# Performance work log

Hardware: AMD Instinct MI355X
Metric: run time of the kernel (lower is better)

The kernel has to match this reference:

```python
import jax, jax.numpy as jnp
import numpy as np

EMBED_DIM = 1024
NUM_HEADS = 16
HEAD_DIM = EMBED_DIM // NUM_HEADS
SCALE = HEAD_DIM ** -0.5


def setup_inputs() -> dict:
    key = jax.random.key(0)
    ks = jax.random.split(key, 12)
    B, S, D = 4, 2048, EMBED_DIM
    x = jax.random.normal(ks[0], (B, S, D), dtype=jnp.float32)
    key_padding_mask = jax.random.randint(ks[1], (B, S), 0, 2).astype(jnp.bool_)
    init = 1.0 / np.sqrt(D)
    def lin(kw, kb):
        W = jax.random.uniform(kw, (D, D), minval=-init, maxval=init, dtype=jnp.float32)
        b = jax.random.uniform(kb, (D,), minval=-init, maxval=init, dtype=jnp.float32)
        return W, b
    Wq, bq = lin(ks[2], ks[3])
    Wk, bk = lin(ks[4], ks[5])
    Wv, bv = lin(ks[6], ks[7])
    Wo, bo = lin(ks[8], ks[9])
    return {"x": x, "key_padding_mask": key_padding_mask,
            "Wq": Wq, "bq": bq, "Wk": Wk, "bk": bk,
            "Wv": Wv, "bv": bv, "Wo": Wo, "bo": bo}


def reference(x, key_padding_mask, Wq, bq, Wk, bk, Wv, bv, Wo, bo):
    B, S, D = x.shape
    H, Hd = NUM_HEADS, HEAD_DIM
    # projections (torch Linear: y = x @ W.T + b)
    q = (x @ Wq.T + bq).reshape(B, S, H, Hd).transpose(0, 2, 1, 3)  # [B,H,S,Hd]
    k = (x @ Wk.T + bk).reshape(B, S, H, Hd).transpose(0, 2, 1, 3)
    v = (x @ Wv.T + bv).reshape(B, S, H, Hd).transpose(0, 2, 1, 3)
    scores = jnp.einsum('bhqd,bhkd->bhqk', q, k) * SCALE  # [B,H,S,S]
    mask = key_padding_mask[:, None, None, :]  # [B,1,1,S]
    scores = jnp.where(mask, -jnp.inf, scores)
    probs = jax.nn.softmax(scores, axis=-1)
    # dropout p=0.0 (inference) -> identity
    out = jnp.einsum('bhqk,bhkd->bhqd', probs, v)  # [B,H,S,Hd]
    out = out.transpose(0, 2, 1, 3).reshape(B, S, D)
    return out @ Wo.T + bo
```

## Files before the change

### kernel.cpp

```cpp
#include <hip/hip_runtime.h>
#include <stdint.h>

typedef __bf16 bf16;
typedef __bf16 bf16x8 __attribute__((ext_vector_type(8)));
typedef float f32x4 __attribute__((ext_vector_type(4)));

#define SEQ 2048
#define NHEAD 16
#define HDIM 64
#define DMODEL 1024
#define NBATCH 4
#define ATT_SCALE 0.18033688011112042f
#define SEQHD (SEQ * HDIM)
#define BHSTRIDE (2 * SEQHD)


__device__ __forceinline__ void gload_lds16(const bf16* g, bf16* l) {
  __builtin_amdgcn_global_load_lds(
      (const __attribute__((address_space(1))) uint32_t*)g,
      (__attribute__((address_space(3))) uint32_t*)l, 16, 0, 0);
}

__device__ __forceinline__ uint32_t pk2(float a, float b) {
  bf16 x = (bf16)a, y = (bf16)b;
  return (uint32_t)__builtin_bit_cast(uint16_t, x) |
         ((uint32_t)__builtin_bit_cast(uint16_t, y) << 16);
}

__global__ __launch_bounds__(256) void cvt_kernel(const float* __restrict__ src,
                                                  bf16* __restrict__ dst) {
  size_t i = ((size_t)blockIdx.x * 256 + threadIdx.x) * 16;
#pragma unroll
  for (int j = 0; j < 2; ++j) {
    float4 f0 = *(const float4*)(src + i + j * 8);
    float4 f1 = *(const float4*)(src + i + j * 8 + 4);
    bf16x8 v;
    v[0] = (bf16)f0.x; v[1] = (bf16)f0.y; v[2] = (bf16)f0.z; v[3] = (bf16)f0.w;
    v[4] = (bf16)f1.x; v[5] = (bf16)f1.y; v[6] = (bf16)f1.z; v[7] = (bf16)f1.w;
    *(bf16x8*)(dst + i + j * 8) = v;
  }
}

__global__ __launch_bounds__(256) void cvt3_kernel(const float* __restrict__ a,
                                                   const float* __restrict__ b,
                                                   const float* __restrict__ c,
                                                   bf16* __restrict__ dst) {
  const float* s = blockIdx.y == 0 ? a : (blockIdx.y == 1 ? b : c);
  bf16* d = dst + (size_t)blockIdx.y * DMODEL * DMODEL;
  size_t i = ((size_t)blockIdx.x * 256 + threadIdx.x) * 16;
#pragma unroll
  for (int j = 0; j < 2; ++j) {
    float4 f0 = *(const float4*)(s + i + j * 8);
    float4 f1 = *(const float4*)(s + i + j * 8 + 4);
    bf16x8 v;
    v[0] = (bf16)f0.x; v[1] = (bf16)f0.y; v[2] = (bf16)f0.z; v[3] = (bf16)f0.w;
    v[4] = (bf16)f1.x; v[5] = (bf16)f1.y; v[6] = (bf16)f1.z; v[7] = (bf16)f1.w;
    *(bf16x8*)(d + i + j * 8) = v;
  }
}

__global__ __launch_bounds__(256) void scan_kernel(int* __restrict__ posv,
                                                   int* __restrict__ inv) {
  __shared__ int sums[256];
  const int b = blockIdx.x, t = threadIdx.x;
  int* m = posv + b * SEQ;
  int* iv = inv + b * SEQ;
  int f[8], cnt = 0;
#pragma unroll
  for (int j = 0; j < 8; ++j) {
    int x = m[t * 8 + j];
    int unm = (x < 0) ? 0 : ((x & 0x40000000) ? 1 : (x == 0 ? 1 : 0));
    f[j] = unm; cnt += unm;
    iv[t * 8 + j] = 0;
  }
  sums[t] = cnt;
  __syncthreads();
  if (t == 0) {
    int acc = 0;
#pragma unroll 8
    for (int i = 0; i < 256; ++i) { int s = sums[i]; sums[i] = acc; acc += s; }
  }
  __syncthreads();
  int p = sums[t];
#pragma unroll
  for (int j = 0; j < 8; ++j) {
    m[t * 8 + j] = (int)((f[j] ? 0x40000000u : 0x80000000u) | (unsigned)p);
    if (f[j]) iv[p] = t * 8 + j;
    p += f[j];
  }
}

__global__ __launch_bounds__(256) void qproj_kernel(
    const bf16* __restrict__ xb, const bf16* __restrict__ Wall,
    const float* __restrict__ bq, bf16* __restrict__ Qall) {
  __shared__ __align__(16) bf16 lW[64 * 64];
  __shared__ __align__(16) bf16 lXw[4][32 * 64];
  const int t = threadIdx.x, wave = t >> 6, lane = t & 63;
  const int quad = lane >> 4, c = lane & 15;
  const int m0 = blockIdx.x * 128;
  const int h = blockIdx.y;
  const bf16* W = Wall + (size_t)(h * HDIM) * DMODEL;
  bf16* pw = lXw[wave];
  const int sr = lane >> 3, sg = lane & 7;
  const bf16* aS = xb + (size_t)(m0 + wave * 32 + sr) * DMODEL + ((sg ^ sr) * 8);
  const bf16* wS = W + (size_t)(wave * 8 + sr) * DMODEL + ((sg ^ sr) * 8);
  f32x4 acc[2][4] = {};
  for (int k0 = 0; k0 < DMODEL; k0 += 64) {
    __syncthreads();
    gload_lds16(wS + k0, lW + wave * 512);
    gload_lds16(wS + 32 * DMODEL + k0, lW + wave * 512 + 2048);
#pragma unroll
    for (int ii = 0; ii < 4; ++ii)
      gload_lds16(aS + k0 + (size_t)ii * 8 * DMODEL, pw + ii * 512);
    __syncthreads();
#pragma unroll
    for (int kk = 0; kk < 2; ++kk) {
      bf16x8 af[2], bfr[4];
#pragma unroll
      for (int mi = 0; mi < 2; ++mi) {
        int row = mi * 16 + c;
        af[mi] = *(const bf16x8*)(pw + row * 64 + (((kk * 4 + quad) ^ (row & 7)) * 8));
      }
#pragma unroll
      for (int ni = 0; ni < 4; ++ni) {
        int row = ni * 16 + c;
        bfr[ni] = *(const bf16x8*)(lW + row * 64 + (((kk * 4 + quad) ^ (row & 7)) * 8));
      }
#pragma unroll
      for (int mi = 0; mi < 2; ++mi)
#pragma unroll
        for (int ni = 0; ni < 4; ++ni)
          acc[mi][ni] = __builtin_amdgcn_mfma_f32_16x16x32_bf16(af[mi], bfr[ni], acc[mi][ni], 0, 0, 0);
    }
  }
#pragma unroll
  for (int ni = 0; ni < 4; ++ni) {
    int hd = ni * 16 + c;
    float bqv = bq[h * HDIM + hd];
#pragma unroll
    for (int mi = 0; mi < 2; ++mi)
#pragma unroll
      for (int r = 0; r < 4; ++r) {
        int tok = m0 + wave * 32 + mi * 16 + quad * 4 + r;
        int b = tok >> 11, s = tok & 2047;
        Qall[((size_t)(b * NHEAD + h) * SEQ + s) * HDIM + hd] =
            (bf16)((acc[mi][ni][r] + bqv) * ATT_SCALE);
      }
  }
}

__global__ __launch_bounds__(256) void kvproj_kernel(
    const bf16* __restrict__ xb, const bf16* __restrict__ Wall,
    const float* __restrict__ bk, const float* __restrict__ bv,
    const int* __restrict__ posv, const int* __restrict__ inv,
    bf16* __restrict__ kv) {
  __shared__ __align__(16) bf16 lW[64 * 64];
  __shared__ __align__(16) bf16 lXw[4][32 * 64];
  const int t = threadIdx.x, wave = t >> 6, lane = t & 63;
  const int quad = lane >> 4, c = lane & 15;
  const int bx = blockIdx.x;
  const int b_loc = bx >> 4, mb = bx & 15;
  const int nt = blockIdx.y;
  const int isV = nt >> 4, h = nt & 15;
  int v2 = posv[b_loc * SEQ + SEQ - 1];
  int nk = (v2 & 0x3FFFFFFF) + (v2 >= 0 ? 1 : 0);
  const int c0 = mb * 128;
  if (c0 >= nk) return;
  const bf16* W = Wall + (size_t)(1 + isV) * DMODEL * DMODEL + (size_t)(h * HDIM) * DMODEL;
  const float* bias = (isV ? bv : bk) + h * HDIM;
  bf16* pw = lXw[wave];
  const int sr = lane >> 3, sg = lane & 7;
  const int swzc = (sg ^ sr) * 8;
  const bf16* wS = W + (size_t)(wave * 8 + sr) * DMODEL + swzc;
  const int* invb = inv + b_loc * SEQ;
  int grow[4];
#pragma unroll
  for (int ii = 0; ii < 4; ++ii)
    grow[ii] = invb[c0 + wave * 32 + ii * 8 + sr];
  const bf16* xbb = xb + (size_t)b_loc * SEQ * DMODEL + swzc;
  f32x4 acc[2][4] = {};
  for (int k0 = 0; k0 < DMODEL; k0 += 64) {
    __syncthreads();
    gload_lds16(wS + k0, lW + wave * 512);
    gload_lds16(wS + 32 * DMODEL + k0, lW + wave * 512 + 2048);
#pragma unroll
    for (int ii = 0; ii < 4; ++ii)
      gload_lds16(xbb + (size_t)grow[ii] * DMODEL + k0, pw + ii * 512);
    __syncthreads();
#pragma unroll
    for (int kk = 0; kk < 2; ++kk) {
      bf16x8 af[2], bfr[4];
#pragma unroll
      for (int mi = 0; mi < 2; ++mi) {
        int row = mi * 16 + c;
        af[mi] = *(const bf16x8*)(pw + row * 64 + (((kk * 4 + quad) ^ (row & 7)) * 8));
      }
#pragma unroll
      for (int ni = 0; ni < 4; ++ni) {
        int row = ni * 16 + c;
        bfr[ni] = *(const bf16x8*)(lW + row * 64 + (((kk * 4 + quad) ^ (row & 7)) * 8));
      }
#pragma unroll
      for (int mi = 0; mi < 2; ++mi)
#pragma unroll
        for (int ni = 0; ni < 4; ++ni)
          acc[mi][ni] = __builtin_amdgcn_mfma_f32_16x16x32_bf16(af[mi], bfr[ni], acc[mi][ni], 0, 0, 0);
    }
  }
  bf16* base = kv + (size_t)(b_loc * NHEAD + h) * BHSTRIDE;
#pragma unroll
  for (int ni = 0; ni < 4; ++ni) {
    int hd = ni * 16 + c;
    float bv_ = bias[hd];
#pragma unroll
    for (int mi = 0; mi < 2; ++mi)
#pragma unroll
      for (int r = 0; r < 4; ++r) {
        int dst = c0 + wave * 32 + mi * 16 + quad * 4 + r;
        float val = acc[mi][ni][r] + bv_;
        if (isV) base[SEQHD + (size_t)hd * SEQ + dst] = (bf16)val;
        else     base[(size_t)dst * HDIM + hd] = (bf16)val;
      }
  }
}

__global__ __launch_bounds__(256) void zf_kernel(bf16* __restrict__ kv,
                                                 const int* __restrict__ posv) {
  const int bh = blockIdx.x, t = threadIdx.x;
  const int b_loc = bh >> 4, h = bh & 15;
  int v2 = posv[b_loc * SEQ + SEQ - 1];
  int nk = (v2 & 0x3FFFFFFF) + (v2 >= 0 ? 1 : 0);
  int NT = ((nk + 63) >> 6) << 6;
  int pad = NT - nk;
  if (pad == 0) return;
  bf16* base = kv + (size_t)(b_loc * NHEAD + h) * BHSTRIDE;
  int hd = t & 63;
  for (int rr = t >> 6; rr < pad; rr += 4) {
    base[(size_t)(nk + rr) * HDIM + hd] = (bf16)0.0f;
    base[SEQHD + (size_t)hd * SEQ + nk + rr] = (bf16)0.0f;
  }
}

__global__ __launch_bounds__(256, 4) void attn4_kernel(
    const bf16* __restrict__ Qall, const bf16* __restrict__ KV,
    const int* __restrict__ posv, bf16* __restrict__ O, int chunk) {
  __shared__ __align__(16) bf16 lK[64 * 64];
  __shared__ __align__(16) bf16 lV[64 * 64];
  __shared__ __align__(16) bf16 lPw[4][16 * 64];
  const int t = threadIdx.x, wave = t >> 6, lane = t & 63;
  const int quad = lane >> 4, c = lane & 15;
  const int i = blockIdx.x;
  const int xcd = i & 7, slot = i >> 3;
  const int bhl = xcd * 4 + (slot >> 5);
  const int qt = slot & 31;
  const int b_loc = bhl >> 4, h = bhl & 15;
  const int b = chunk * 2 + b_loc;
  const int q0 = qt * 64 + wave * 16;
  const bf16* Qh = Qall + (size_t)(b * NHEAD + h) * SEQHD;
  const bf16* Kb = KV + (size_t)(b_loc * NHEAD + h) * BHSTRIDE;
  const bf16* Vtb = Kb + SEQHD;
  bf16* pw = lPw[wave];

  int v2 = posv[b * SEQ + SEQ - 1];
  int nk = (v2 & 0x3FFFFFFF) + (v2 >= 0 ? 1 : 0);
  int NT = ((nk + 63) >> 6) << 6;

  const int srow = t >> 3;
  const int sswz = (t & 7) ^ (srow & 7);
  const bf16* kSrc = Kb + (size_t)srow * HDIM + sswz * 8;
  const bf16* vSrc = Vtb + (size_t)srow * SEQ + sswz * 8;
  bf16* kDst = lK + wave * 512;
  bf16* vDst = lV + wave * 512;

  bf16x8 qf[2];
#pragma unroll
  for (int kk = 0; kk < 2; ++kk)
    qf[kk] = *(const bf16x8*)(Qh + (size_t)(q0 + c) * HDIM + kk * 32 + quad * 8);

  f32x4 oacc[4] = {};
  float mrun = -1e30f, lrun = 0.0f;

  const int pbase = c * 64 + (quad & 1) * 4;
  const int pswz = c & 7;

#pragma unroll
  for (int i2 = 0; i2 < 2; ++i2) {
    gload_lds16(kSrc + i2 * 32 * HDIM, kDst + i2 * 2048);
    gload_lds16(vSrc + (size_t)i2 * 32 * SEQ, vDst + i2 * 2048);
  }
  __syncthreads();

  for (int kt = 0; kt < NT; kt += 64) {
    f32x4 sacc[4] = {};
#pragma unroll
    for (int kk = 0; kk < 2; ++kk) {
      bf16x8 kf[4];
#pragma unroll
      for (int ni = 0; ni < 4; ++ni) {
        int row = ni * 16 + c;
        kf[ni] = *(const bf16x8*)(lK + row * 64 + (((kk * 4 + quad) ^ (row & 7)) * 8));
      }
#pragma unroll
      for (int ni = 0; ni < 4; ++ni)
        sacc[ni] = __builtin_amdgcn_mfma_f32_16x16x32_bf16(kf[ni], qf[kk], sacc[ni], 0, 0, 0);
    }

    __syncthreads();
    if (kt + 64 < NT) {
      const bf16* ks = kSrc + (size_t)(kt + 64) * HDIM;
#pragma unroll
      for (int i2 = 0; i2 < 2; ++i2) gload_lds16(ks + i2 * 32 * HDIM, kDst + i2 * 2048);
    }

    if (kt + 64 > nk) {
      int base = kt + quad * 4 - nk;
#pragma unroll
      for (int ni = 0; ni < 4; ++ni)
#pragma unroll
        for (int r = 0; r < 4; ++r)
          if (base + ni * 16 + r >= 0) sacc[ni][r] = -3e38f;
    }

    float m1 = fmaxf(fmaxf(sacc[0][0], sacc[0][1]), sacc[0][2]);
    float m2 = fmaxf(fmaxf(sacc[0][3], sacc[1][0]), sacc[1][1]);
    float m3 = fmaxf(fmaxf(sacc[1][2], sacc[1][3]), sacc[2][0]);
    float m4 = fmaxf(fmaxf(sacc[2][1], sacc[2][2]), sacc[2][3]);
    float m5 = fmaxf(fmaxf(sacc[3][0], sacc[3][1]), sacc[3][2]);
    float mx = fmaxf(fmaxf(fmaxf(m1, m2), m3), fmaxf(fmaxf(m4, m5), sacc[3][3]));
    mx = fmaxf(mx, __shfl_xor(mx, 16));
    mx = fmaxf(mx, __shfl_xor(mx, 32));

    if (!__all(mx - mrun <= 8.0f)) {
      float mn = fmaxf(mrun, mx);
      float al = __builtin_amdgcn_exp2f(mrun - mn);
      mrun = mn;
      lrun *= al;
      float al4[4];
#pragma unroll
      for (int r = 0; r < 4; ++r) al4[r] = __shfl(al, quad * 4 + r);
#pragma unroll
      for (int ni = 0; ni < 4; ++ni)
#pragma unroll
        for (int r = 0; r < 4; ++r) oacc[ni][r] *= al4[r];
    }

    float rs = 0.0f;
#pragma unroll
    for (int ni = 0; ni < 4; ++ni)
#pragma unroll
      for (int r = 0; r < 4; ++r) {
        float e = __builtin_amdgcn_exp2f(sacc[ni][r] - mrun);
        sacc[ni][r] = e; rs += e;
      }
    rs += __shfl_xor(rs, 16);
    rs += __shfl_xor(rs, 32);
    lrun += rs;

#pragma unroll
    for (int ni = 0; ni < 4; ++ni) {
      uint2 u;
      u.x = pk2(sacc[ni][0], sacc[ni][1]);
      u.y = pk2(sacc[ni][2], sacc[ni][3]);
      int sl = pbase + (((ni * 2 + (quad >> 1)) ^ pswz) * 8);
      *(uint2*)(pw + sl) = u;
    }

#pragma unroll
    for (int kk = 0; kk < 2; ++kk) {
      bf16x8 pf, vfr[4];
      pf = *(const bf16x8*)(pw + c * 64 + (((kk * 4 + quad) ^ (c & 7)) * 8));
#pragma unroll
      for (int ni = 0; ni < 4; ++ni) {
        int row = ni * 16 + c;
        vfr[ni] = *(const bf16x8*)(lV + row * 64 + (((kk * 4 + quad) ^ (row & 7)) * 8));
      }
#pragma unroll
      for (int ni = 0; ni < 4; ++ni)
        oacc[ni] = __builtin_amdgcn_mfma_f32_16x16x32_bf16(pf, vfr[ni], oacc[ni], 0, 0, 0);
    }

    __syncthreads();
    if (kt + 64 < NT) {
      const bf16* vs = vSrc + (kt + 64);
#pragma unroll
      for (int i2 = 0; i2 < 2; ++i2) gload_lds16(vs + (size_t)i2 * 32 * SEQ, vDst + i2 * 2048);
    }
  }

  float linv = lrun > 0.0f ? 1.0f / lrun : 0.0f;
  float linv4[4];
#pragma unroll
  for (int r = 0; r < 4; ++r) linv4[r] = __shfl(linv, quad * 4 + r);
#pragma unroll
  for (int r = 0; r < 4; ++r) {
    size_t tok = (size_t)b * SEQ + q0 + quad * 4 + r;
#pragma unroll
    for (int ni = 0; ni < 4; ++ni)
      O[tok * DMODEL + h * HDIM + ni * 16 + c] = (bf16)(oacc[ni][r] * linv4[r]);
  }
}

__global__ __launch_bounds__(256) void outproj_kernel(
    const bf16* __restrict__ O, const bf16* __restrict__ Wob,
    const float* __restrict__ bo, float* __restrict__ out) {
  __shared__ __align__(16) bf16 lW[64 * 64];
  __shared__ __align__(16) bf16 lXw[4][32 * 64];
  const int t = threadIdx.x, wave = t >> 6, lane = t & 63;
  const int quad = lane >> 4, c = lane & 15;
  const int m0 = blockIdx.x * 128;
  const int n0 = blockIdx.y * 64;
  bf16* pw = lXw[wave];
  const int sr = lane >> 3, sg = lane & 7;
  const bf16* aS = O + (size_t)(m0 + wave * 32 + sr) * DMODEL + ((sg ^ sr) * 8);
  const bf16* wS = Wob + (size_t)(n0 + wave * 8 + sr) * DMODEL + ((sg ^ sr) * 8);
  f32x4 acc[2][4] = {};
  for (int k0 = 0; k0 < DMODEL; k0 += 64) {
    __syncthreads();
    gload_lds16(wS + k0, lW + wave * 512);
    gload_lds16(wS + 32 * DMODEL + k0, lW + wave * 512 + 2048);
#pragma unroll
    for (int ii = 0; ii < 4; ++ii)
      gload_lds16(aS + k0 + (size_t)ii * 8 * DMODEL, pw + ii * 512);
    __syncthreads();
#pragma unroll
    for (int kk = 0; kk < 2; ++kk) {
      bf16x8 af[2], bfr[4];
#pragma unroll
      for (int mi = 0; mi < 2; ++mi) {
        int row = mi * 16 + c;
        af[mi] = *(const bf16x8*)(pw + row * 64 + (((kk * 4 + quad) ^ (row & 7)) * 8));
      }
#pragma unroll
      for (int ni = 0; ni < 4; ++ni) {
        int row = ni * 16 + c;
        bfr[ni] = *(const bf16x8*)(lW + row * 64 + (((kk * 4 + quad) ^ (row & 7)) * 8));
      }
#pragma unroll
      for (int mi = 0; mi < 2; ++mi)
#pragma unroll
        for (int ni = 0; ni < 4; ++ni)
          acc[mi][ni] = __builtin_amdgcn_mfma_f32_16x16x32_bf16(af[mi], bfr[ni], acc[mi][ni], 0, 0, 0);
    }
  }
#pragma unroll
  for (int ni = 0; ni < 4; ++ni) {
    int gn = n0 + ni * 16 + c;
    float bv_ = bo[gn];
#pragma unroll
    for (int mi = 0; mi < 2; ++mi)
#pragma unroll
      for (int r = 0; r < 4; ++r) {
        int gm = m0 + wave * 32 + mi * 16 + quad * 4 + r;
        out[(size_t)gm * DMODEL + gn] = acc[mi][ni][r] + bv_;
      }
  }
}

extern "C" void kernel_launch(void* const* d_in, const int* in_sizes, int n_in,
                              void* d_out, int out_size, void* d_ws, size_t ws_size,
                              hipStream_t stream) {
  const float* x  = (const float*)d_in[0];
  int*         posv = (int*)d_in[1];
  const float* Wq = (const float*)d_in[2]; const float* bq = (const float*)d_in[3];
  const float* Wk = (const float*)d_in[4]; const float* bk = (const float*)d_in[5];
  const float* Wv = (const float*)d_in[6]; const float* bv = (const float*)d_in[7];
  const float* Wo = (const float*)d_in[8]; const float* bo = (const float*)d_in[9];
  float* out = (float*)d_out;
  char* outc = (char*)d_out;
  char* xc   = (char*)d_in[0];
  const size_t half = (size_t)NBATCH * SEQ * DMODEL * 2;
  const size_t qtr  = half / 2;

  bf16* Qall = (bf16*)d_out;
  bf16* xbf  = (bf16*)(outc + half);
  bf16* KV   = (bf16*)xc;
  bf16* O    = (bf16*)(xc + half);
  bf16* Wbf3 = (bf16*)(xc + half + qtr);
  int*  inv  = (int*)(xc + half + qtr + (size_t)3 * DMODEL * DMODEL * 2);
  bf16* Wobf = (bf16*)xc;

  cvt_kernel<<<dim3(2048), 256, 0, stream>>>(x, xbf);
  scan_kernel<<<dim3(NBATCH), 256, 0, stream>>>(posv, inv);
  cvt3_kernel<<<dim3(256, 3), 256, 0, stream>>>(Wq, Wk, Wv, Wbf3);
  qproj_kernel<<<dim3(64, 16), 256, 0, stream>>>(xbf, Wbf3, bq, Qall);
  kvproj_kernel<<<dim3(32, 32), 256, 0, stream>>>(xbf, Wbf3, bk, bv, posv, inv, KV);
  zf_kernel<<<dim3(32), 256, 0, stream>>>(KV, posv);
  attn4_kernel<<<dim3(1024), 256, 0, stream>>>(Qall, KV, posv, O, 0);
  kvproj_kernel<<<dim3(32, 32), 256, 0, stream>>>(xbf + (size_t)2 * SEQ * DMODEL, Wbf3, bk, bv,
                                                  posv + 2 * SEQ, inv + 2 * SEQ, KV);
  zf_kernel<<<dim3(32), 256, 0, stream>>>(KV, posv + 2 * SEQ);
  attn4_kernel<<<dim3(1024), 256, 0, stream>>>(Qall, KV, posv, O, 1);
  cvt_kernel<<<dim3(256), 256, 0, stream>>>(Wo, Wobf);
  outproj_kernel<<<dim3(64, 16), 256, 0, stream>>>(O, Wobf, bo, out);
}
```

Before: 298.1 us.

## Double-buffer K/V tiles in attention and fuse small prep/zero-fill kernels

Each attention tile now has two LDS buffers for K and V. The next tile's loads are issued at the top of the iteration, and one barrier per iteration replaces two, so global-to-LDS copies overlap with both MFMA phases. The weight-convert and mask-scan kernels are merged into one launch. The padding zero-fill kernel is removed by having the KV projection write zeros for rows past nk. LDS use per block doubles for K/V, which may affect occupancy at 4 blocks per CU. Whether kvproj covers every padded row the old zero-fill handled is not verifiable from the visible code.

After: 287.8 us. -3.4%, faster.

```diff
diff --git a/kernel.cpp b/kernel.cpp
--- a/kernel.cpp
+++ b/kernel.cpp
@@ -41,28 +41,28 @@
   }
 }
 
-__global__ __launch_bounds__(256) void cvt3_kernel(const float* __restrict__ a,
-                                                   const float* __restrict__ b,
-                                                   const float* __restrict__ c,
-                                                   bf16* __restrict__ dst) {
-  const float* s = blockIdx.y == 0 ? a : (blockIdx.y == 1 ? b : c);
-  bf16* d = dst + (size_t)blockIdx.y * DMODEL * DMODEL;
-  size_t i = ((size_t)blockIdx.x * 256 + threadIdx.x) * 16;
-#pragma unroll
-  for (int j = 0; j < 2; ++j) {
-    float4 f0 = *(const float4*)(s + i + j * 8);
-    float4 f1 = *(const float4*)(s + i + j * 8 + 4);
-    bf16x8 v;
-    v[0] = (bf16)f0.x; v[1] = (bf16)f0.y; v[2] = (bf16)f0.z; v[3] = (bf16)f0.w;
-    v[4] = (bf16)f1.x; v[5] = (bf16)f1.y; v[6] = (bf16)f1.z; v[7] = (bf16)f1.w;
-    *(bf16x8*)(d + i + j * 8) = v;
-  }
-}
-
-__global__ __launch_bounds__(256) void scan_kernel(int* __restrict__ posv,
-                                                   int* __restrict__ inv) {
+__global__ __launch_bounds__(256) void prep_kernel(
+    const float* __restrict__ Wq, const float* __restrict__ Wk,
+    const float* __restrict__ Wv, bf16* __restrict__ Wbf3,
+    int* __restrict__ posv, int* __restrict__ inv) {
   __shared__ int sums[256];
-  const int b = blockIdx.x, t = threadIdx.x;
+  const int bx = blockIdx.x, t = threadIdx.x;
+  if (bx < 768) {
+    const float* s = bx < 256 ? Wq : (bx < 512 ? Wk : Wv);
+    bf16* d = Wbf3 + (size_t)(bx >> 8) * DMODEL * DMODEL;
+    size_t i = ((size_t)(bx & 255) * 256 + t) * 16;
+#pragma unroll
+    for (int j = 0; j < 2; ++j) {
+      float4 f0 = *(const float4*)(s + i + j * 8);
+      float4 f1 = *(const float4*)(s + i + j * 8 + 4);
+      bf16x8 v;
+      v[0] = (bf16)f0.x; v[1] = (bf16)f0.y; v[2] = (bf16)f0.z; v[3] = (bf16)f0.w;
+      v[4] = (bf16)f1.x; v[5] = (bf16)f1.y; v[6] = (bf16)f1.z; v[7] = (bf16)f1.w;
+      *(bf16x8*)(d + i + j * 8) = v;
+    }
+    return;
+  }
+  const int b = bx - 768;
   int* m = posv + b * SEQ;
   int* iv = inv + b * SEQ;
   int f[8], cnt = 0;
@@ -217,35 +217,18 @@
 #pragma unroll
       for (int r = 0; r < 4; ++r) {
         int dst = c0 + wave * 32 + mi * 16 + quad * 4 + r;
-        float val = acc[mi][ni][r] + bv_;
+        float val = (dst < nk) ? (acc[mi][ni][r] + bv_) : 0.0f;
         if (isV) base[SEQHD + (size_t)hd * SEQ + dst] = (bf16)val;
         else     base[(size_t)dst * HDIM + hd] = (bf16)val;
       }
-  }
-}
-
-__global__ __launch_bounds__(256) void zf_kernel(bf16* __restrict__ kv,
-                                                 const int* __restrict__ posv) {
-  const int bh = blockIdx.x, t = threadIdx.x;
-  const int b_loc = bh >> 4, h = bh & 15;
-  int v2 = posv[b_loc * SEQ + SEQ - 1];
-  int nk = (v2 & 0x3FFFFFFF) + (v2 >= 0 ? 1 : 0);
-  int NT = ((nk + 63) >> 6) << 6;
-  int pad = NT - nk;
-  if (pad == 0) return;
-  bf16* base = kv + (size_t)(b_loc * NHEAD + h) * BHSTRIDE;
-  int hd = t & 63;
-  for (int rr = t >> 6; rr < pad; rr += 4) {
-    base[(size_t)(nk + rr) * HDIM + hd] = (bf16)0.0f;
-    base[SEQHD + (size_t)hd * SEQ + nk + rr] = (bf16)0.0f;
   }
 }
 
 __global__ __launch_bounds__(256, 4) void attn4_kernel(
     const bf16* __restrict__ Qall, const bf16* __restrict__ KV,
     const int* __restrict__ posv, bf16* __restrict__ O, int chunk) {
-  __shared__ __align__(16) bf16 lK[64 * 64];
-  __shared__ __align__(16) bf16 lV[64 * 64];
+  __shared__ __align__(16) bf16 lK[2][64 * 64];
+  __shared__ __align__(16) bf16 lV[2][64 * 64];
   __shared__ __align__(16) bf16 lPw[4][16 * 64];
   const int t = threadIdx.x, wave = t >> 6, lane = t & 63;
   const int quad = lane >> 4, c = lane & 15;
@@ -269,8 +252,7 @@
   const int sswz = (t & 7) ^ (srow & 7);
   const bf16* kSrc = Kb + (size_t)srow * HDIM + sswz * 8;
   const bf16* vSrc = Vtb + (size_t)srow * SEQ + sswz * 8;
-  bf16* kDst = lK + wave * 512;
-  bf16* vDst = lV + wave * 512;
+  const int sOff = wave * 512;
 
   bf16x8 qf[2];
 #pragma unroll
@@ -285,12 +267,27 @@
 
 #pragma unroll
   for (int i2 = 0; i2 < 2; ++i2) {
-    gload_lds16(kSrc + i2 * 32 * HDIM, kDst + i2 * 2048);
-    gload_lds16(vSrc + (size_t)i2 * 32 * SEQ, vDst + i2 * 2048);
+    gload_lds16(kSrc + i2 * 32 * HDIM, &lK[0][0] + sOff + i2 * 2048);
+    gload_lds16(vSrc + (size_t)i2 * 32 * SEQ, &lV[0][0] + sOff + i2 * 2048);
   }
   __syncthreads();
 
-  for (int kt = 0; kt < NT; kt += 64) {
+  int idx = 0;
+  for (int kt = 0; kt < NT; kt += 64, idx ^= 1) {
+    if (kt + 64 < NT) {
+      const bf16* ks = kSrc + (size_t)(kt + 64) * HDIM;
+      const bf16* vs = vSrc + (kt + 64);
+      bf16* kD = &lK[0][0] + (idx ^ 1) * 4096 + sOff;
+      bf16* vD = &lV[0][0] + (idx ^ 1) * 4096 + sOff;
+#pragma unroll
+      for (int i2 = 0; i2 < 2; ++i2) {
+        gload_lds16(ks + i2 * 32 * HDIM, kD + i2 * 2048);
+        gload_lds16(vs + (size_t)i2 * 32 * SEQ, vD + i2 * 2048);
+      }
+    }
+    const bf16* lKc = &lK[0][0] + idx * 4096;
+    const bf16* lVc = &lV[0][0] + idx * 4096;
+
     f32x4 sacc[4] = {};
 #pragma unroll
     for (int kk = 0; kk < 2; ++kk) {
@@ -298,18 +295,11 @@
 #pragma unroll
       for (int ni = 0; ni < 4; ++ni) {
         int row = ni * 16 + c;
-        kf[ni] = *(const bf16x8*)(lK + row * 64 + (((kk * 4 + quad) ^ (row & 7)) * 8));
+        kf[ni] = *(const bf16x8*)(lKc + row * 64 + (((kk * 4 + quad) ^ (row & 7)) * 8));
       }
 #pragma unroll
       for (int ni = 0; ni < 4; ++ni)
         sacc[ni] = __builtin_amdgcn_mfma_f32_16x16x32_bf16(kf[ni], qf[kk], sacc[ni], 0, 0, 0);
-    }
-
-    __syncthreads();
-    if (kt + 64 < NT) {
-      const bf16* ks = kSrc + (size_t)(kt + 64) * HDIM;
-#pragma unroll
-      for (int i2 = 0; i2 < 2; ++i2) gload_lds16(ks + i2 * 32 * HDIM, kDst + i2 * 2048);
     }
 
     if (kt + 64 > nk) {
@@ -372,7 +362,7 @@
 #pragma unroll
       for (int ni = 0; ni < 4; ++ni) {
         int row = ni * 16 + c;
-        vfr[ni] = *(const bf16x8*)(lV + row * 64 + (((kk * 4 + quad) ^ (row & 7)) * 8));
+        vfr[ni] = *(const bf16x8*)(lVc + row * 64 + (((kk * 4 + quad) ^ (row & 7)) * 8));
       }
 #pragma unroll
       for (int ni = 0; ni < 4; ++ni)
@@ -380,11 +370,6 @@
     }
 
     __syncthreads();
-    if (kt + 64 < NT) {
-      const bf16* vs = vSrc + (kt + 64);
-#pragma unroll
-      for (int i2 = 0; i2 < 2; ++i2) gload_lds16(vs + (size_t)i2 * 32 * SEQ, vDst + i2 * 2048);
-    }
   }
 
   float linv = lrun > 0.0f ? 1.0f / lrun : 0.0f;
@@ -480,15 +465,12 @@
   bf16* Wobf = (bf16*)xc;
 
   cvt_kernel<<<dim3(2048), 256, 0, stream>>>(x, xbf);
-  scan_kernel<<<dim3(NBATCH), 256, 0, stream>>>(posv, inv);
-  cvt3_kernel<<<dim3(256, 3), 256, 0, stream>>>(Wq, Wk, Wv, Wbf3);
+  prep_kernel<<<dim3(772), 256, 0, stream>>>(Wq, Wk, Wv, Wbf3, posv, inv);
   qproj_kernel<<<dim3(64, 16), 256, 0, stream>>>(xbf, Wbf3, bq, Qall);
   kvproj_kernel<<<dim3(32, 32), 256, 0, stream>>>(xbf, Wbf3, bk, bv, posv, inv, KV);
-  zf_kernel<<<dim3(32), 256, 0, stream>>>(KV, posv);
   attn4_kernel<<<dim3(1024), 256, 0, stream>>>(Qall, KV, posv, O, 0);
   kvproj_kernel<<<dim3(32, 32), 256, 0, stream>>>(xbf + (size_t)2 * SEQ * DMODEL, Wbf3, bk, bv,
                                                   posv + 2 * SEQ, inv + 2 * SEQ, KV);
-  zf_kernel<<<dim3(32), 256, 0, stream>>>(KV, posv + 2 * SEQ);
   attn4_kernel<<<dim3(1024), 256, 0, stream>>>(Qall, KV, posv, O, 1);
   cvt_kernel<<<dim3(256), 256, 0, stream>>>(Wo, Wobf);
   outproj_kernel<<<dim3(64, 16), 256, 0, stream>>>(O, Wobf, bo, out);
```
